# Kernel tuning notes

Hardware: AMD Instinct MI355X
Metric: run time of the kernel (lower is better)

The kernel has to match this reference:

```python
import jax, jax.numpy as jnp
import numpy as np

B, N, S, K = 8, 4096, 1024, 128   # clouds, pts/cloud, fps samples (ratio=0.25), max neighbors
R = 0.2                            # radius
DIN = 3                            # point feature dim


def setup_inputs() -> dict:
    key = jax.random.key(0)
    ks = jax.random.split(key, 8)
    x = jax.random.normal(ks[0], (B * N, DIN), dtype=jnp.float32)
    pos = jax.random.uniform(ks[1], (B * N, 3), dtype=jnp.float32)
    batch = jnp.repeat(jnp.arange(B, dtype=jnp.int32), N)
    def lin(k, fi, fo):
        return jax.random.normal(k, (fi, fo), dtype=jnp.float32) / np.float32(np.sqrt(fi))
    W1 = lin(ks[2], DIN + 3, 64); b1 = jnp.zeros((64,), jnp.float32)
    W2 = lin(ks[3], 64, 64);      b2 = jnp.zeros((64,), jnp.float32)
    W3 = lin(ks[4], 64, 128);     b3 = jnp.zeros((128,), jnp.float32)
    return {"x": x, "pos": pos, "W1": W1, "b1": b1, "W2": W2, "b2": b2,
            "W3": W3, "b3": b3, "batch": batch}


def _fps(pos3):
    """Farthest point sampling per cloud. pos3: [B,N,3] -> idx [B,S] (start at point 0)."""
    d0 = jnp.sum((pos3 - pos3[:, :1]) ** 2, axis=-1)  # [B,N]
    def step(min_d, _):
        nxt = jnp.argmax(min_d, axis=1).astype(jnp.int32)             # [B]
        p = jnp.take_along_axis(pos3, nxt[:, None, None], axis=1)      # [B,1,3]
        d = jnp.sum((pos3 - p) ** 2, axis=-1)
        return jnp.minimum(min_d, d), nxt
    _, idxs = jax.lax.scan(step, d0, None, length=S - 1)               # [S-1,B]
    first = jnp.zeros((B, 1), jnp.int32)
    return jnp.concatenate([first, idxs.T], axis=1)                    # [B,S]


def reference(x, pos, W1, b1, W2, b2, W3, b3, batch):
    x3 = x.reshape(B, N, DIN)
    pos3 = pos.reshape(B, N, 3)
    batch2 = batch.reshape(B, N)

    idx = _fps(pos3)                                                   # [B,S]
    q = jnp.take_along_axis(pos3, idx[:, :, None], axis=1)             # [B,S,3]

    # radius ball query, capped at K nearest within R (deterministic variant of torch radius)
    d2 = jnp.sum((q[:, :, None, :] - pos3[:, None, :, :]) ** 2, -1)    # [B,S,N]
    masked = jnp.where(d2 <= R * R, d2, jnp.inf)
    negd, nbr = jax.lax.top_k(-masked, K)                              # [B,S,K]
    valid = jnp.isfinite(negd)                                         # [B,S,K]

    gather = jax.vmap(lambda a, i: a[i])                                # per-cloud fancy gather
    xj = gather(x3, nbr)                                               # [B,S,K,DIN]
    pj = gather(pos3, nbr)                                             # [B,S,K,3]
    rel = pj - q[:, :, None, :]
    feat = jnp.concatenate([xj, rel], axis=-1)                         # [B,S,K,6]

    h = jax.nn.relu(feat @ W1 + b1)
    h = jax.nn.relu(h @ W2 + b2)
    h = h @ W3 + b3                                                    # plain last layer

    h = jnp.where(valid[..., None], h, -jnp.inf)
    out = jnp.max(h, axis=2)                                           # max aggregation [B,S,128]
    out = jnp.where(jnp.any(valid, axis=2)[..., None], out, 0.0)

    x_out = out.reshape(B * S, -1)
    pos_out = q.reshape(B * S, 3)
    batch_out = jnp.take_along_axis(batch2, idx, axis=1).reshape(B * S)
    return x_out, pos_out, batch_out
```

## Files before the change

### kernel.cpp

```cpp
#include <hip/hip_runtime.h>
#include <hip/hip_fp16.h>

#define BB   8
#define NPTS 4096
#define SS   1024
#define KK   128

typedef _Float16 half8 __attribute__((ext_vector_type(8)));
typedef float    f32x4 __attribute__((ext_vector_type(4)));

#define FPS_T 256
#define PPT   16

#define DPP_FMAX(CTRL)                                                                  \
    {                                                                                   \
        unsigned o = (unsigned)__builtin_amdgcn_update_dpp(                             \
            (int)__float_as_uint(m), (int)__float_as_uint(m), CTRL, 0xF, 0xF, false);   \
        m = fmaxf(m, __uint_as_float(o));                                               \
    }

__global__ __launch_bounds__(FPS_T) void fps_e_kernel(const float* __restrict__ pos,
                                                      const int* __restrict__ batch,
                                                      const float* __restrict__ x,
                                                      const float* __restrict__ W1,
                                                      float* __restrict__ E,
                                                      float* __restrict__ pos_out,
                                                      float* __restrict__ batch_out) {
    if (blockIdx.x >= BB) {
        int id = (blockIdx.x - BB) * FPS_T + threadIdx.x;
        int c = id & 63;
        int n = id >> 6;
        float x0 = x[n * 3 + 0], x1 = x[n * 3 + 1], x2 = x[n * 3 + 2];
        float p0 = pos[n * 3 + 0], p1 = pos[n * 3 + 1], p2 = pos[n * 3 + 2];
        float v = x0 * W1[0 * 64 + c] + x1 * W1[1 * 64 + c] + x2 * W1[2 * 64 + c]
                + p0 * W1[3 * 64 + c] + p1 * W1[4 * 64 + c] + p2 * W1[5 * 64 + c];
        E[(size_t)n * 64 + c] = v;
        return;
    }

    __shared__ __align__(16) float4 Pl[NPTS];
    __shared__ __align__(16) unsigned long long wkey[2][4];

    int b = blockIdx.x;
    int t = threadIdx.x;
    int w = t >> 6, l = t & 63;
    const float* P = pos + (size_t)b * NPTS * 3;

    for (int i = t; i < NPTS; i += FPS_T) {
        Pl[i] = make_float4(P[i * 3 + 0], P[i * 3 + 1], P[i * 3 + 2], 0.f);
    }
    float bval = (float)batch[(size_t)b * NPTS];
    for (int i = t; i < SS; i += FPS_T) batch_out[b * SS + i] = bval;

    float px[PPT], py[PPT], pz[PPT], md[PPT];
    int base = t * PPT;
#pragma unroll
    for (int j = 0; j < PPT; j++) {
        px[j] = P[(base + j) * 3 + 0];
        py[j] = P[(base + j) * 3 + 1];
        pz[j] = P[(base + j) * 3 + 2];
    }
    float c0x = P[0], c0y = P[1], c0z = P[2];
    float lm = -1.f;
#pragma unroll
    for (int j = 0; j < PPT; j++) {
        float dx = __fsub_rn(px[j], c0x);
        float dy = __fsub_rn(py[j], c0y);
        float dz = __fsub_rn(pz[j], c0z);
        md[j] = __fadd_rn(__fadd_rn(__fmul_rn(dx, dx), __fmul_rn(dy, dy)), __fmul_rn(dz, dz));
        lm = fmaxf(lm, md[j]);
    }
    if (t == 0) {
        float* qp = pos_out + (size_t)(b * SS) * 3;
        qp[0] = c0x; qp[1] = c0y; qp[2] = c0z;
    }
    __syncthreads();

    for (int s = 1; s < SS; s++) {
        int jsel = 0x7FFFFFFF;
#pragma unroll
        for (int j = PPT - 1; j >= 0; j--)
            if (md[j] == lm) jsel = base + j;

        float m = lm;
        DPP_FMAX(0x111)
        DPP_FMAX(0x112)
        DPP_FMAX(0x114)
        DPP_FMAX(0x118)
        DPP_FMAX(0x142)
        DPP_FMAX(0x143)
        float wm = __uint_as_float((unsigned)__builtin_amdgcn_readlane(__float_as_uint(m), 63));

        unsigned long long mask = __ballot(lm == wm);
        int L = __ffsll((long long)mask) - 1;
        int si = __builtin_amdgcn_readlane(jsel, L);

        if (l == 0)
            wkey[s & 1][w] = (((unsigned long long)__float_as_uint(wm)) << 32) | (~(unsigned)si);
        __syncthreads();

        const unsigned long long* wk = wkey[s & 1];
        unsigned long long g0 = wk[0] > wk[1] ? wk[0] : wk[1];
        unsigned long long g1 = wk[2] > wk[3] ? wk[2] : wk[3];
        unsigned long long g = g0 > g1 ? g0 : g1;
        int gi = (int)(~(unsigned)g);

        float4 c = Pl[gi];
        if (t == 0) {
            float* qp = pos_out + (size_t)(b * SS + s) * 3;
            qp[0] = c.x; qp[1] = c.y; qp[2] = c.z;
        }
        float nlm = -1.f;
#pragma unroll
        for (int j = 0; j < PPT; j++) {
            float dx = __fsub_rn(px[j], c.x);
            float dy = __fsub_rn(py[j], c.y);
            float dz = __fsub_rn(pz[j], c.z);
            float d2 = __fadd_rn(__fadd_rn(__fmul_rn(dx, dx), __fmul_rn(dy, dy)), __fmul_rn(dz, dz));
            md[j] = fminf(md[j], d2);
            nlm = fmaxf(nlm, md[j]);
        }
        lm = nlm;
    }
}

#define CAP 512

__global__ __launch_bounds__(256) void ball_kernel(const float* __restrict__ pos,
                                                   const float* __restrict__ qpos,
                                                   int* __restrict__ nbr) {
    __shared__ float cd2[4][CAP];
    __shared__ int   cidx[4][CAP];
    int t = threadIdx.x, w = t >> 6, l = t & 63;
    int qi = blockIdx.x * 4 + w;
    int b = qi >> 10;
    int bBase = b * NPTS;
    const float* P = pos + (size_t)bBase * 3;
    float qx = qpos[qi * 3 + 0], qy = qpos[qi * 3 + 1], qz = qpos[qi * 3 + 2];

    int total = 0;
    for (int n0 = 0; n0 < NPTS; n0 += 64) {
        int n = n0 + l;
        float x = P[n * 3 + 0], y = P[n * 3 + 1], z = P[n * 3 + 2];
        float dx = __fsub_rn(qx, x);
        float dy = __fsub_rn(qy, y);
        float dz = __fsub_rn(qz, z);
        float d2 = __fadd_rn(__fadd_rn(__fmul_rn(dx, dx), __fmul_rn(dy, dy)), __fmul_rn(dz, dz));
        bool in = (d2 <= 0.04f);
        unsigned long long mask = __ballot(in);
        int mypos = total + (int)__popcll(mask & ((1ull << l) - 1ull));
        if (in && mypos < CAP) { cd2[w][mypos] = d2; cidx[w][mypos] = n; }
        total += (int)__popcll(mask);
    }

    int* onbr = nbr + (size_t)qi * KK;
    if (total <= KK) {
        for (int i = l; i < KK; i += 64)
            onbr[i] = bBase + cidx[w][i < total ? i : 0];
    } else {
        int nc = total < CAP ? total : CAP;
        unsigned long long key[8];
#pragma unroll
        for (int i = 0; i < 8; i++) {
            int p = l + (i << 6);
            key[i] = (p < nc)
                   ? ((((unsigned long long)__float_as_uint(cd2[w][p])) << 12) | (unsigned)cidx[w][p])
                   : ~0ull;
        }
        unsigned long long lo = 0, hi = ((unsigned long long)0x3D23D70Bu) << 12;
        while (lo < hi) {
            unsigned long long mid = (lo + hi) >> 1;
            int cnt = 0;
#pragma unroll
            for (int i = 0; i < 8; i++) cnt += (int)__popcll(__ballot(key[i] <= mid));
            if (cnt >= KK) hi = mid; else lo = mid + 1;
        }
        int done = 0;
#pragma unroll
        for (int i = 0; i < 8; i++) {
            bool s2 = (key[i] <= lo);
            unsigned long long mk = __ballot(s2);
            int p2 = done + (int)__popcll(mk & ((1ull << l) - 1ull));
            if (s2) onbr[p2] = bBase + (int)(key[i] & 0xFFFull);
            done += (int)__popcll(mk);
        }
    }
}

__global__ __launch_bounds__(256) void mlp_kernel(const float* __restrict__ E,
                                                  const int* __restrict__ nbr,
                                                  const float* __restrict__ qpos,
                                                  const float* __restrict__ W1,
                                                  const float* __restrict__ b1,
                                                  const float* __restrict__ W2,
                                                  const float* __restrict__ b2,
                                                  const float* __restrict__ W3,
                                                  const float* __restrict__ b3,
                                                  float* __restrict__ xout,
                                                  int qPerBlk) {
    __shared__ __align__(16) _Float16 W2t[64 * 64];
    __shared__ __align__(16) _Float16 W3t[128 * 64];
    __shared__ __align__(16) _Float16 h2buf[4][32 * 64];
    __shared__ __align__(16) float csh[64];
    __shared__ float cpart[4][128];
    __shared__ float b2s[64];
    __shared__ float b3s[128];

    int t = threadIdx.x, w = t >> 6, l = t & 63;
    int lhi = l >> 4, llo = l & 15;

    for (int i = t; i < 64 * 64; i += 256) {
        int n = i >> 6, k = i & 63;
        W2t[(n << 6) | (k ^ ((n & 7) << 3))] = (_Float16)W2[k * 64 + n];
    }
    for (int i = t; i < 128 * 64; i += 256) {
        int n = i >> 6, k = i & 63;
        W3t[(n << 6) | (k ^ ((n & 7) << 3))] = (_Float16)W3[k * 128 + n];
    }
    if (t < 64) b2s[t] = b2[t];
    if (t < 128) b3s[t] = b3[t];
    __syncthreads();

    int q0 = blockIdx.x * qPerBlk;
    for (int qq = 0; qq < qPerBlk; qq++) {
        int qi = q0 + qq;
        if (t < 64) {
            float qx = qpos[qi * 3 + 0], qy = qpos[qi * 3 + 1], qz = qpos[qi * 3 + 2];
            csh[t] = b1[t] - (qx * W1[3 * 64 + t] + qy * W1[4 * 64 + t] + qz * W1[5 * 64 + t]);
        }
        __syncthreads();

        half8 a2[2][2];
        int row0 = w * 32;
#pragma unroll
        for (int mt = 0; mt < 2; mt++) {
            int r = row0 + mt * 16 + llo;
            int nb = nbr[(size_t)qi * KK + r];
            const float* Er = E + (size_t)nb * 64;
#pragma unroll
            for (int ks = 0; ks < 2; ks++) {
                int k0 = lhi * 8 + ks * 32;
                f32x4 e0 = *(const f32x4*)(Er + k0);
                f32x4 e1 = *(const f32x4*)(Er + k0 + 4);
                f32x4 c0 = *(const f32x4*)(csh + k0);
                f32x4 c1 = *(const f32x4*)(csh + k0 + 4);
                half8 a;
#pragma unroll
                for (int e = 0; e < 4; e++) {
                    a[e]     = (_Float16)fmaxf(e0[e] + c0[e], 0.f);
                    a[4 + e] = (_Float16)fmaxf(e1[e] + c1[e], 0.f);
                }
                a2[mt][ks] = a;
            }
        }

        f32x4 acc2[2][4];
#pragma unroll
        for (int mt = 0; mt < 2; mt++)
#pragma unroll
            for (int nt = 0; nt < 4; nt++) acc2[mt][nt] = (f32x4){0.f, 0.f, 0.f, 0.f};
#pragma unroll
        for (int ks = 0; ks < 2; ks++) {
            int k0 = lhi * 8 + ks * 32;
#pragma unroll
            for (int nt = 0; nt < 4; nt++) {
                int n = nt * 16 + llo;
                half8 bf = *(const half8*)&W2t[(n << 6) | (k0 ^ ((n & 7) << 3))];
#pragma unroll
                for (int mt = 0; mt < 2; mt++)
                    acc2[mt][nt] = __builtin_amdgcn_mfma_f32_16x16x32_f16(a2[mt][ks], bf, acc2[mt][nt], 0, 0, 0);
            }
        }

        _Float16* hb = h2buf[w];
#pragma unroll
        for (int mt = 0; mt < 2; mt++)
#pragma unroll
            for (int nt = 0; nt < 4; nt++)
#pragma unroll
                for (int r = 0; r < 4; r++) {
                    int lr = mt * 16 + lhi * 4 + r;
                    int n = nt * 16 + llo;
                    float v = fmaxf(acc2[mt][nt][r] + b2s[n], 0.f);
                    hb[(lr << 6) | (n ^ ((lr & 7) << 3))] = (_Float16)v;
                }

        half8 a3[2][2];
#pragma unroll
        for (int mt = 0; mt < 2; mt++)
#pragma unroll
            for (int ks = 0; ks < 2; ks++) {
                int lr = mt * 16 + llo;
                int k0 = lhi * 8 + ks * 32;
                a3[mt][ks] = *(const half8*)&hb[(lr << 6) | (k0 ^ ((lr & 7) << 3))];
            }
        f32x4 acc3[2][8];
#pragma unroll
        for (int mt = 0; mt < 2; mt++)
#pragma unroll
            for (int nt = 0; nt < 8; nt++) acc3[mt][nt] = (f32x4){0.f, 0.f, 0.f, 0.f};
#pragma unroll
        for (int ks = 0; ks < 2; ks++) {
            int k0 = lhi * 8 + ks * 32;
#pragma unroll
            for (int nt = 0; nt < 8; nt++) {
                int n = nt * 16 + llo;
                half8 bf = *(const half8*)&W3t[(n << 6) | (k0 ^ ((n & 7) << 3))];
#pragma unroll
                for (int mt = 0; mt < 2; mt++)
                    acc3[mt][nt] = __builtin_amdgcn_mfma_f32_16x16x32_f16(a3[mt][ks], bf, acc3[mt][nt], 0, 0, 0);
            }
        }

#pragma unroll
        for (int nt = 0; nt < 8; nt++) {
            float m = acc3[0][nt][0];
#pragma unroll
            for (int r = 1; r < 4; r++) m = fmaxf(m, acc3[0][nt][r]);
#pragma unroll
            for (int r = 0; r < 4; r++) m = fmaxf(m, acc3[1][nt][r]);
            m = fmaxf(m, __shfl_xor(m, 16));
            m = fmaxf(m, __shfl_xor(m, 32));
            if (l < 16) cpart[w][nt * 16 + l] = m;
        }
        __syncthreads();
        if (t < 128) {
            float v = fmaxf(fmaxf(cpart[0][t], cpart[1][t]), fmaxf(cpart[2][t], cpart[3][t])) + b3s[t];
            xout[(size_t)qi * 128 + t] = v;
        }
        __syncthreads();
    }
}

extern "C" void kernel_launch(void* const* d_in, const int* in_sizes, int n_in,
                              void* d_out, int out_size, void* d_ws, size_t ws_size,
                              hipStream_t stream) {
    const float* x   = (const float*)d_in[0];
    const float* pos = (const float*)d_in[1];
    const float* W1  = (const float*)d_in[2];
    const float* b1  = (const float*)d_in[3];
    const float* W2  = (const float*)d_in[4];
    const float* b2  = (const float*)d_in[5];
    const float* W3  = (const float*)d_in[6];
    const float* b3  = (const float*)d_in[7];
    const int* batch = (const int*)d_in[8];

    float* xout      = (float*)d_out;
    float* pos_out   = xout + (size_t)BB * SS * 128;
    float* batch_out = pos_out + (size_t)BB * SS * 3;

    float* E  = (float*)d_ws;
    int* nbr  = (int*)((char*)d_ws + (size_t)32768 * 64 * 4);

    fps_e_kernel<<<dim3(BB + 8192), dim3(FPS_T), 0, stream>>>(pos, batch, x, W1, E, pos_out, batch_out);
    ball_kernel<<<dim3(2048), dim3(256), 0, stream>>>(pos, pos_out, nbr);
    mlp_kernel<<<dim3(2048), dim3(256), 0, stream>>>(E, nbr, pos_out, W1, b1, W2, b2, W3, b3, xout, 4);
}
```

Baseline: 725.0 us.

## Fuse FPS, ball query and MLP into one persistent kernel with progress flags

Merges the three kernels into a single persistent launch. Eight high-priority blocks run farthest point sampling and publish per-cloud progress counters every 64 samples. The remaining worker blocks compute the E table, then run the ball query and MLP for each query group once its FPS samples are published. This lets the neighbor search and MLP overlap with the long serial FPS loop and drops the intermediate neighbor buffer. It relies on all blocks being co-resident for the spin-waits, which risks deadlock if they are not, and it adds atomic polling overhead.

```diff
diff --git a/kernel.cpp b/kernel.cpp
--- a/kernel.cpp
+++ b/kernel.cpp
@@ -1,16 +1,43 @@
 #include <hip/hip_runtime.h>
 #include <hip/hip_fp16.h>
 
-#define BB   8
-#define NPTS 4096
-#define SS   1024
-#define KK   128
+#define BB    8
+#define NPTS  4096
+#define SS    1024
+#define KK    128
+#define CAP   512
+#define NW    504
+#define TPB   256
+#define PPT   16
 
 typedef _Float16 half8 __attribute__((ext_vector_type(8)));
 typedef float    f32x4 __attribute__((ext_vector_type(4)));
 
-#define FPS_T 256
-#define PPT   16
+
+struct __align__(16) FpsSm {
+    float4 Pl[NPTS];
+    unsigned long long wkey[2][4];
+};
+struct __align__(16) WkSm {
+    float cd2[4][CAP];
+    int   cidx[4][CAP];
+    int   nbrL[4][KK];
+    _Float16 W2t[64 * 64];
+    _Float16 W3t[128 * 64];
+    _Float16 h2buf[4][32 * 64];
+    float csh[64];
+    float cpart[4][128];
+    float b2s[64];
+    float b3s[128];
+};
+union __align__(16) SMem { FpsSm f; WkSm w; };
+
+__device__ __forceinline__ void st_rel(unsigned* p, unsigned v) {
+    __hip_atomic_store(p, v, __ATOMIC_RELEASE, __HIP_MEMORY_SCOPE_AGENT);
+}
+__device__ __forceinline__ unsigned ld_acq(unsigned* p) {
+    return __hip_atomic_load(p, __ATOMIC_ACQUIRE, __HIP_MEMORY_SCOPE_AGENT);
+}
 
 #define DPP_FMAX(CTRL)                                                                  \
     {                                                                                   \
@@ -19,15 +46,110 @@
         m = fmaxf(m, __uint_as_float(o));                                               \
     }
 
-__global__ __launch_bounds__(FPS_T) void fps_e_kernel(const float* __restrict__ pos,
-                                                      const int* __restrict__ batch,
-                                                      const float* __restrict__ x,
-                                                      const float* __restrict__ W1,
-                                                      float* __restrict__ E,
-                                                      float* __restrict__ pos_out,
-                                                      float* __restrict__ batch_out) {
-    if (blockIdx.x >= BB) {
-        int id = (blockIdx.x - BB) * FPS_T + threadIdx.x;
+__global__ __launch_bounds__(TPB) void fused_kernel(const float* __restrict__ pos,
+                                                    const int* __restrict__ batch,
+                                                    const float* __restrict__ x,
+                                                    const float* __restrict__ W1,
+                                                    const float* __restrict__ b1,
+                                                    const float* __restrict__ W2,
+                                                    const float* __restrict__ b2,
+                                                    const float* __restrict__ W3,
+                                                    const float* __restrict__ b3,
+                                                    float* __restrict__ E,
+                                                    float* __restrict__ pos_out,
+                                                    float* __restrict__ batch_out,
+                                                    float* __restrict__ xout,
+                                                    unsigned* __restrict__ sync) {
+    __shared__ SMem sm;
+    int t = threadIdx.x, w = t >> 6, l = t & 63;
+
+    if (blockIdx.x < BB) {
+        __builtin_amdgcn_s_setprio(3);
+        int b = blockIdx.x;
+        const float* P = pos + (size_t)b * NPTS * 3;
+
+        for (int i = t; i < NPTS; i += TPB) {
+            sm.f.Pl[i] = make_float4(P[i * 3 + 0], P[i * 3 + 1], P[i * 3 + 2], 0.f);
+        }
+        float bval = (float)batch[(size_t)b * NPTS];
+        for (int i = t; i < SS; i += TPB) batch_out[b * SS + i] = bval;
+
+        float px[PPT], py[PPT], pz[PPT], md[PPT];
+        int base = t * PPT;
+#pragma unroll
+        for (int j = 0; j < PPT; j++) {
+            px[j] = P[(base + j) * 3 + 0];
+            py[j] = P[(base + j) * 3 + 1];
+            pz[j] = P[(base + j) * 3 + 2];
+        }
+        float c0x = P[0], c0y = P[1], c0z = P[2];
+        float lm = -1.f;
+#pragma unroll
+        for (int j = 0; j < PPT; j++) {
+            float dx = __fsub_rn(px[j], c0x);
+            float dy = __fsub_rn(py[j], c0y);
+            float dz = __fsub_rn(pz[j], c0z);
+            md[j] = __fadd_rn(__fadd_rn(__fmul_rn(dx, dx), __fmul_rn(dy, dy)), __fmul_rn(dz, dz));
+            lm = fmaxf(lm, md[j]);
+        }
+        if (t == 0) {
+            float* qp = pos_out + (size_t)(b * SS) * 3;
+            qp[0] = c0x; qp[1] = c0y; qp[2] = c0z;
+        }
+        __syncthreads();
+
+        for (int s = 1; s < SS; s++) {
+            int jsel = 0x7FFFFFFF;
+#pragma unroll
+            for (int j = PPT - 1; j >= 0; j--)
+                if (md[j] == lm) jsel = base + j;
+
+            float m = lm;
+            DPP_FMAX(0x111)
+            DPP_FMAX(0x112)
+            DPP_FMAX(0x114)
+            DPP_FMAX(0x118)
+            DPP_FMAX(0x142)
+            DPP_FMAX(0x143)
+            float wm = __uint_as_float((unsigned)__builtin_amdgcn_readlane(__float_as_uint(m), 63));
+
+            unsigned long long mask = __ballot(lm == wm);
+            int L = __ffsll((long long)mask) - 1;
+            int si = __builtin_amdgcn_readlane(jsel, L);
+
+            if (l == 0)
+                sm.f.wkey[s & 1][w] = (((unsigned long long)__float_as_uint(wm)) << 32) | (~(unsigned)si);
+            __syncthreads();
+
+            const unsigned long long* wk = sm.f.wkey[s & 1];
+            unsigned long long g0 = wk[0] > wk[1] ? wk[0] : wk[1];
+            unsigned long long g1 = wk[2] > wk[3] ? wk[2] : wk[3];
+            unsigned long long g = g0 > g1 ? g0 : g1;
+            int gi = (int)(~(unsigned)g);
+
+            float4 c = sm.f.Pl[gi];
+            if (t == 0) {
+                float* qp = pos_out + (size_t)(b * SS + s) * 3;
+                qp[0] = c.x; qp[1] = c.y; qp[2] = c.z;
+                if ((s & 63) == 63) st_rel(&sync[b * 32], (unsigned)(s + 1));
+            }
+#pragma unroll
+            for (int j = 0; j < PPT; j++) {
+                float dx = __fsub_rn(px[j], c.x);
+                float dy = __fsub_rn(py[j], c.y);
+                float dz = __fsub_rn(pz[j], c.z);
+                float d2 = __fadd_rn(__fadd_rn(__fmul_rn(dx, dx), __fmul_rn(dy, dy)), __fmul_rn(dz, dz));
+                md[j] = fminf(md[j], d2);
+                lm = (j == 0) ? fmaxf(-1.f, md[0]) : fmaxf(lm, md[j]);
+            }
+        }
+        return;
+    }
+
+    int wid = blockIdx.x - BB;
+    unsigned* ectr = &sync[256];
+
+    for (int id = wid * TPB + t; id < 32768 * 64; id += NW * TPB) {
         int c = id & 63;
         int n = id >> 6;
         float x0 = x[n * 3 + 0], x1 = x[n * 3 + 1], x2 = x[n * 3 + 2];
@@ -35,298 +157,198 @@
         float v = x0 * W1[0 * 64 + c] + x1 * W1[1 * 64 + c] + x2 * W1[2 * 64 + c]
                 + p0 * W1[3 * 64 + c] + p1 * W1[4 * 64 + c] + p2 * W1[5 * 64 + c];
         E[(size_t)n * 64 + c] = v;
-        return;
-    }
-
-    __shared__ __align__(16) float4 Pl[NPTS];
-    __shared__ __align__(16) unsigned long long wkey[2][4];
-
-    int b = blockIdx.x;
-    int t = threadIdx.x;
-    int w = t >> 6, l = t & 63;
-    const float* P = pos + (size_t)b * NPTS * 3;
-
-    for (int i = t; i < NPTS; i += FPS_T) {
-        Pl[i] = make_float4(P[i * 3 + 0], P[i * 3 + 1], P[i * 3 + 2], 0.f);
-    }
-    float bval = (float)batch[(size_t)b * NPTS];
-    for (int i = t; i < SS; i += FPS_T) batch_out[b * SS + i] = bval;
-
-    float px[PPT], py[PPT], pz[PPT], md[PPT];
-    int base = t * PPT;
-#pragma unroll
-    for (int j = 0; j < PPT; j++) {
-        px[j] = P[(base + j) * 3 + 0];
-        py[j] = P[(base + j) * 3 + 1];
-        pz[j] = P[(base + j) * 3 + 2];
-    }
-    float c0x = P[0], c0y = P[1], c0z = P[2];
-    float lm = -1.f;
-#pragma unroll
-    for (int j = 0; j < PPT; j++) {
-        float dx = __fsub_rn(px[j], c0x);
-        float dy = __fsub_rn(py[j], c0y);
-        float dz = __fsub_rn(pz[j], c0z);
-        md[j] = __fadd_rn(__fadd_rn(__fmul_rn(dx, dx), __fmul_rn(dy, dy)), __fmul_rn(dz, dz));
-        lm = fmaxf(lm, md[j]);
-    }
+    }
+    if (l == 0) __hip_atomic_fetch_add(ectr, 1u, __ATOMIC_RELEASE, __HIP_MEMORY_SCOPE_AGENT);
+
+    for (int i = t; i < 64 * 64; i += TPB) {
+        int n = i >> 6, k = i & 63;
+        sm.w.W2t[(n << 6) | (k ^ ((n & 7) << 3))] = (_Float16)W2[k * 64 + n];
+    }
+    for (int i = t; i < 128 * 64; i += TPB) {
+        int n = i >> 6, k = i & 63;
+        sm.w.W3t[(n << 6) | (k ^ ((n & 7) << 3))] = (_Float16)W3[k * 128 + n];
+    }
+    if (t < 64) sm.w.b2s[t] = b2[t];
+    if (t < 128) sm.w.b3s[t] = b3[t];
+
     if (t == 0) {
-        float* qp = pos_out + (size_t)(b * SS) * 3;
-        qp[0] = c0x; qp[1] = c0y; qp[2] = c0z;
+        while (ld_acq(ectr) < NW * 4u) __builtin_amdgcn_s_sleep(16);
     }
     __syncthreads();
 
-    for (int s = 1; s < SS; s++) {
-        int jsel = 0x7FFFFFFF;
-#pragma unroll
-        for (int j = PPT - 1; j >= 0; j--)
-            if (md[j] == lm) jsel = base + j;
-
-        float m = lm;
-        DPP_FMAX(0x111)
-        DPP_FMAX(0x112)
-        DPP_FMAX(0x114)
-        DPP_FMAX(0x118)
-        DPP_FMAX(0x142)
-        DPP_FMAX(0x143)
-        float wm = __uint_as_float((unsigned)__builtin_amdgcn_readlane(__float_as_uint(m), 63));
-
-        unsigned long long mask = __ballot(lm == wm);
-        int L = __ffsll((long long)mask) - 1;
-        int si = __builtin_amdgcn_readlane(jsel, L);
-
-        if (l == 0)
-            wkey[s & 1][w] = (((unsigned long long)__float_as_uint(wm)) << 32) | (~(unsigned)si);
+    int lhi = l >> 4, llo = l & 15;
+
+    for (int g = wid; g < 2048; g += NW) {
+        int cb = g >> 8;
+        unsigned need = ((unsigned)(g & 255)) * 4u + 4u;
+        if (t == 0) {
+            while (ld_acq(&sync[cb * 32]) < need) __builtin_amdgcn_s_sleep(16);
+        }
         __syncthreads();
 
-        const unsigned long long* wk = wkey[s & 1];
-        unsigned long long g0 = wk[0] > wk[1] ? wk[0] : wk[1];
-        unsigned long long g1 = wk[2] > wk[3] ? wk[2] : wk[3];
-        unsigned long long g = g0 > g1 ? g0 : g1;
-        int gi = (int)(~(unsigned)g);
-
-        float4 c = Pl[gi];
-        if (t == 0) {
-            float* qp = pos_out + (size_t)(b * SS + s) * 3;
-            qp[0] = c.x; qp[1] = c.y; qp[2] = c.z;
-        }
-        float nlm = -1.f;
-#pragma unroll
-        for (int j = 0; j < PPT; j++) {
-            float dx = __fsub_rn(px[j], c.x);
-            float dy = __fsub_rn(py[j], c.y);
-            float dz = __fsub_rn(pz[j], c.z);
-            float d2 = __fadd_rn(__fadd_rn(__fmul_rn(dx, dx), __fmul_rn(dy, dy)), __fmul_rn(dz, dz));
-            md[j] = fminf(md[j], d2);
-            nlm = fmaxf(nlm, md[j]);
-        }
-        lm = nlm;
-    }
-}
-
-#define CAP 512
-
-__global__ __launch_bounds__(256) void ball_kernel(const float* __restrict__ pos,
-                                                   const float* __restrict__ qpos,
-                                                   int* __restrict__ nbr) {
-    __shared__ float cd2[4][CAP];
-    __shared__ int   cidx[4][CAP];
-    int t = threadIdx.x, w = t >> 6, l = t & 63;
-    int qi = blockIdx.x * 4 + w;
-    int b = qi >> 10;
-    int bBase = b * NPTS;
-    const float* P = pos + (size_t)bBase * 3;
-    float qx = qpos[qi * 3 + 0], qy = qpos[qi * 3 + 1], qz = qpos[qi * 3 + 2];
-
-    int total = 0;
-    for (int n0 = 0; n0 < NPTS; n0 += 64) {
-        int n = n0 + l;
-        float x = P[n * 3 + 0], y = P[n * 3 + 1], z = P[n * 3 + 2];
-        float dx = __fsub_rn(qx, x);
-        float dy = __fsub_rn(qy, y);
-        float dz = __fsub_rn(qz, z);
-        float d2 = __fadd_rn(__fadd_rn(__fmul_rn(dx, dx), __fmul_rn(dy, dy)), __fmul_rn(dz, dz));
-        bool in = (d2 <= 0.04f);
-        unsigned long long mask = __ballot(in);
-        int mypos = total + (int)__popcll(mask & ((1ull << l) - 1ull));
-        if (in && mypos < CAP) { cd2[w][mypos] = d2; cidx[w][mypos] = n; }
-        total += (int)__popcll(mask);
-    }
-
-    int* onbr = nbr + (size_t)qi * KK;
-    if (total <= KK) {
-        for (int i = l; i < KK; i += 64)
-            onbr[i] = bBase + cidx[w][i < total ? i : 0];
-    } else {
-        int nc = total < CAP ? total : CAP;
-        unsigned long long key[8];
-#pragma unroll
-        for (int i = 0; i < 8; i++) {
-            int p = l + (i << 6);
-            key[i] = (p < nc)
-                   ? ((((unsigned long long)__float_as_uint(cd2[w][p])) << 12) | (unsigned)cidx[w][p])
-                   : ~0ull;
-        }
-        unsigned long long lo = 0, hi = ((unsigned long long)0x3D23D70Bu) << 12;
-        while (lo < hi) {
-            unsigned long long mid = (lo + hi) >> 1;
-            int cnt = 0;
-#pragma unroll
-            for (int i = 0; i < 8; i++) cnt += (int)__popcll(__ballot(key[i] <= mid));
-            if (cnt >= KK) hi = mid; else lo = mid + 1;
-        }
-        int done = 0;
-#pragma unroll
-        for (int i = 0; i < 8; i++) {
-            bool s2 = (key[i] <= lo);
-            unsigned long long mk = __ballot(s2);
-            int p2 = done + (int)__popcll(mk & ((1ull << l) - 1ull));
-            if (s2) onbr[p2] = bBase + (int)(key[i] & 0xFFFull);
-            done += (int)__popcll(mk);
-        }
-    }
-}
-
-__global__ __launch_bounds__(256) void mlp_kernel(const float* __restrict__ E,
-                                                  const int* __restrict__ nbr,
-                                                  const float* __restrict__ qpos,
-                                                  const float* __restrict__ W1,
-                                                  const float* __restrict__ b1,
-                                                  const float* __restrict__ W2,
-                                                  const float* __restrict__ b2,
-                                                  const float* __restrict__ W3,
-                                                  const float* __restrict__ b3,
-                                                  float* __restrict__ xout,
-                                                  int qPerBlk) {
-    __shared__ __align__(16) _Float16 W2t[64 * 64];
-    __shared__ __align__(16) _Float16 W3t[128 * 64];
-    __shared__ __align__(16) _Float16 h2buf[4][32 * 64];
-    __shared__ __align__(16) float csh[64];
-    __shared__ float cpart[4][128];
-    __shared__ float b2s[64];
-    __shared__ float b3s[128];
-
-    int t = threadIdx.x, w = t >> 6, l = t & 63;
-    int lhi = l >> 4, llo = l & 15;
-
-    for (int i = t; i < 64 * 64; i += 256) {
-        int n = i >> 6, k = i & 63;
-        W2t[(n << 6) | (k ^ ((n & 7) << 3))] = (_Float16)W2[k * 64 + n];
-    }
-    for (int i = t; i < 128 * 64; i += 256) {
-        int n = i >> 6, k = i & 63;
-        W3t[(n << 6) | (k ^ ((n & 7) << 3))] = (_Float16)W3[k * 128 + n];
-    }
-    if (t < 64) b2s[t] = b2[t];
-    if (t < 128) b3s[t] = b3[t];
-    __syncthreads();
-
-    int q0 = blockIdx.x * qPerBlk;
-    for (int qq = 0; qq < qPerBlk; qq++) {
-        int qi = q0 + qq;
-        if (t < 64) {
-            float qx = qpos[qi * 3 + 0], qy = qpos[qi * 3 + 1], qz = qpos[qi * 3 + 2];
-            csh[t] = b1[t] - (qx * W1[3 * 64 + t] + qy * W1[4 * 64 + t] + qz * W1[5 * 64 + t]);
+        {
+            int qi = 4 * g + w;
+            int bBase = cb * NPTS;
+            const float* P = pos + (size_t)bBase * 3;
+            float qx = pos_out[qi * 3 + 0], qy = pos_out[qi * 3 + 1], qz = pos_out[qi * 3 + 2];
+
+            int total = 0;
+            for (int n0 = 0; n0 < NPTS; n0 += 64) {
+                int n = n0 + l;
+                float xx = P[n * 3 + 0], yy = P[n * 3 + 1], zz = P[n * 3 + 2];
+                float dx = __fsub_rn(qx, xx);
+                float dy = __fsub_rn(qy, yy);
+                float dz = __fsub_rn(qz, zz);
+                float d2 = __fadd_rn(__fadd_rn(__fmul_rn(dx, dx), __fmul_rn(dy, dy)), __fmul_rn(dz, dz));
+                bool in = (d2 <= 0.04f);
+                unsigned long long mask = __ballot(in);
+                int mypos = total + (int)__popcll(mask & ((1ull << l) - 1ull));
+                if (in && mypos < CAP) { sm.w.cd2[w][mypos] = d2; sm.w.cidx[w][mypos] = n; }
+                total += (int)__popcll(mask);
+            }
+
+            if (total <= KK) {
+                for (int i = l; i < KK; i += 64)
+                    sm.w.nbrL[w][i] = bBase + sm.w.cidx[w][i < total ? i : 0];
+            } else {
+                int nc = total < CAP ? total : CAP;
+                unsigned long long key[8];
+#pragma unroll
+                for (int i = 0; i < 8; i++) {
+                    int p = l + (i << 6);
+                    key[i] = (p < nc)
+                           ? ((((unsigned long long)__float_as_uint(sm.w.cd2[w][p])) << 12) | (unsigned)sm.w.cidx[w][p])
+                           : ~0ull;
+                }
+                unsigned long long lo = 0, hi = ((unsigned long long)0x3D23D70Bu) << 12;
+                while (lo < hi) {
+                    unsigned long long mid = (lo + hi) >> 1;
+                    int cnt = 0;
+#pragma unroll
+                    for (int i = 0; i < 8; i++) cnt += (int)__popcll(__ballot(key[i] <= mid));
+                    if (cnt >= KK) hi = mid; else lo = mid + 1;
+                }
+                int done = 0;
+#pragma unroll
+                for (int i = 0; i < 8; i++) {
+                    bool s2 = (key[i] <= lo);
+                    unsigned long long mk = __ballot(s2);
+                    int p2 = done + (int)__popcll(mk & ((1ull << l) - 1ull));
+                    if (s2) sm.w.nbrL[w][p2] = bBase + (int)(key[i] & 0xFFFull);
+                    done += (int)__popcll(mk);
+                }
+            }
         }
         __syncthreads();
 
-        half8 a2[2][2];
-        int row0 = w * 32;
-#pragma unroll
-        for (int mt = 0; mt < 2; mt++) {
-            int r = row0 + mt * 16 + llo;
-            int nb = nbr[(size_t)qi * KK + r];
-            const float* Er = E + (size_t)nb * 64;
+        for (int qq = 0; qq < 4; qq++) {
+            int qi = 4 * g + qq;
+            if (t < 64) {
+                float qx = pos_out[qi * 3 + 0], qy = pos_out[qi * 3 + 1], qz = pos_out[qi * 3 + 2];
+                sm.w.csh[t] = b1[t] - (qx * W1[3 * 64 + t] + qy * W1[4 * 64 + t] + qz * W1[5 * 64 + t]);
+            }
+            __syncthreads();
+
+            half8 a2[2][2];
+            int row0 = w * 32;
+#pragma unroll
+            for (int mt = 0; mt < 2; mt++) {
+                int r = row0 + mt * 16 + llo;
+                int nb = sm.w.nbrL[qq][r];
+                const float* Er = E + (size_t)nb * 64;
+#pragma unroll
+                for (int ks = 0; ks < 2; ks++) {
+                    int k0 = lhi * 8 + ks * 32;
+                    f32x4 e0 = *(const f32x4*)(Er + k0);
+                    f32x4 e1 = *(const f32x4*)(Er + k0 + 4);
+                    f32x4 c0 = *(const f32x4*)(sm.w.csh + k0);
+                    f32x4 c1 = *(const f32x4*)(sm.w.csh + k0 + 4);
+                    half8 a;
+#pragma unroll
+                    for (int e = 0; e < 4; e++) {
+                        a[e]     = (_Float16)fmaxf(e0[e] + c0[e], 0.f);
+                        a[4 + e] = (_Float16)fmaxf(e1[e] + c1[e], 0.f);
+                    }
+                    a2[mt][ks] = a;
+                }
+            }
+
+            f32x4 acc2[2][4];
+#pragma unroll
+            for (int mt = 0; mt < 2; mt++)
+#pragma unroll
+                for (int nt = 0; nt < 4; nt++) acc2[mt][nt] = (f32x4){0.f, 0.f, 0.f, 0.f};
 #pragma unroll
             for (int ks = 0; ks < 2; ks++) {
                 int k0 = lhi * 8 + ks * 32;
-                f32x4 e0 = *(const f32x4*)(Er + k0);
-                f32x4 e1 = *(const f32x4*)(Er + k0 + 4);
-                f32x4 c0 = *(const f32x4*)(csh + k0);
-                f32x4 c1 = *(const f32x4*)(csh + k0 + 4);
-                half8 a;
-#pragma unroll
-                for (int e = 0; e < 4; e++) {
-                    a[e]     = (_Float16)fmaxf(e0[e] + c0[e], 0.f);
-                    a[4 + e] = (_Float16)fmaxf(e1[e] + c1[e], 0.f);
-                }
-                a2[mt][ks] = a;
-            }
-        }
-
-        f32x4 acc2[2][4];
-#pragma unroll
-        for (int mt = 0; mt < 2; mt++)
-#pragma unroll
-            for (int nt = 0; nt < 4; nt++) acc2[mt][nt] = (f32x4){0.f, 0.f, 0.f, 0.f};
-#pragma unroll
-        for (int ks = 0; ks < 2; ks++) {
-            int k0 = lhi * 8 + ks * 32;
-#pragma unroll
-            for (int nt = 0; nt < 4; nt++) {
-                int n = nt * 16 + llo;
-                half8 bf = *(const half8*)&W2t[(n << 6) | (k0 ^ ((n & 7) << 3))];
-#pragma unroll
-                for (int mt = 0; mt < 2; mt++)
-                    acc2[mt][nt] = __builtin_amdgcn_mfma_f32_16x16x32_f16(a2[mt][ks], bf, acc2[mt][nt], 0, 0, 0);
-            }
-        }
-
-        _Float16* hb = h2buf[w];
-#pragma unroll
-        for (int mt = 0; mt < 2; mt++)
-#pragma unroll
-            for (int nt = 0; nt < 4; nt++)
-#pragma unroll
-                for (int r = 0; r < 4; r++) {
-                    int lr = mt * 16 + lhi * 4 + r;
+#pragma unroll
+                for (int nt = 0; nt < 4; nt++) {
                     int n = nt * 16 + llo;
-                    float v = fmaxf(acc2[mt][nt][r] + b2s[n], 0.f);
-                    hb[(lr << 6) | (n ^ ((lr & 7) << 3))] = (_Float16)v;
-                }
-
-        half8 a3[2][2];
-#pragma unroll
-        for (int mt = 0; mt < 2; mt++)
+                    half8 bf = *(const half8*)&sm.w.W2t[(n << 6) | (k0 ^ ((n & 7) << 3))];
+#pragma unroll
+                    for (int mt = 0; mt < 2; mt++)
+                        acc2[mt][nt] = __builtin_amdgcn_mfma_f32_16x16x32_f16(a2[mt][ks], bf, acc2[mt][nt], 0, 0, 0);
+                }
+            }
+
+            _Float16* hb = sm.w.h2buf[w];
+#pragma unroll
+            for (int mt = 0; mt < 2; mt++)
+#pragma unroll
+                for (int nt = 0; nt < 4; nt++)
+#pragma unroll
+                    for (int r = 0; r < 4; r++) {
+                        int lr = mt * 16 + lhi * 4 + r;
+                        int n = nt * 16 + llo;
+                        float v = fmaxf(acc2[mt][nt][r] + sm.w.b2s[n], 0.f);
+                        hb[(lr << 6) | (n ^ ((lr & 7) << 3))] = (_Float16)v;
+                    }
+
+            half8 a3[2][2];
+#pragma unroll
+            for (int mt = 0; mt < 2; mt++)
+#pragma unroll
+                for (int ks = 0; ks < 2; ks++) {
+                    int lr = mt * 16 + llo;
+                    int k0 = lhi * 8 + ks * 32;
+                    a3[mt][ks] = *(const half8*)&hb[(lr << 6) | (k0 ^ ((lr & 7) << 3))];
+                }
+            f32x4 acc3[2][8];
+#pragma unroll
+            for (int mt = 0; mt < 2; mt++)
+#pragma unroll
+                for (int nt = 0; nt < 8; nt++) acc3[mt][nt] = (f32x4){0.f, 0.f, 0.f, 0.f};
 #pragma unroll
             for (int ks = 0; ks < 2; ks++) {
-                int lr = mt * 16 + llo;
                 int k0 = lhi * 8 + ks * 32;
-                a3[mt][ks] = *(const half8*)&hb[(lr << 6) | (k0 ^ ((lr & 7) << 3))];
-            }
-        f32x4 acc3[2][8];
-#pragma unroll
-        for (int mt = 0; mt < 2; mt++)
-#pragma unroll
-            for (int nt = 0; nt < 8; nt++) acc3[mt][nt] = (f32x4){0.f, 0.f, 0.f, 0.f};
-#pragma unroll
-        for (int ks = 0; ks < 2; ks++) {
-            int k0 = lhi * 8 + ks * 32;
+#pragma unroll
+                for (int nt = 0; nt < 8; nt++) {
+                    int n = nt * 16 + llo;
+                    half8 bf = *(const half8*)&sm.w.W3t[(n << 6) | (k0 ^ ((n & 7) << 3))];
+#pragma unroll
+                    for (int mt = 0; mt < 2; mt++)
+                        acc3[mt][nt] = __builtin_amdgcn_mfma_f32_16x16x32_f16(a3[mt][ks], bf, acc3[mt][nt], 0, 0, 0);
+                }
+            }
+
 #pragma unroll
             for (int nt = 0; nt < 8; nt++) {
-                int n = nt * 16 + llo;
-                half8 bf = *(const half8*)&W3t[(n << 6) | (k0 ^ ((n & 7) << 3))];
-#pragma unroll
-                for (int mt = 0; mt < 2; mt++)
-                    acc3[mt][nt] = __builtin_amdgcn_mfma_f32_16x16x32_f16(a3[mt][ks], bf, acc3[mt][nt], 0, 0, 0);
-            }
-        }
-
-#pragma unroll
-        for (int nt = 0; nt < 8; nt++) {
-            float m = acc3[0][nt][0];
-#pragma unroll
-            for (int r = 1; r < 4; r++) m = fmaxf(m, acc3[0][nt][r]);
-#pragma unroll
-            for (int r = 0; r < 4; r++) m = fmaxf(m, acc3[1][nt][r]);
-            m = fmaxf(m, __shfl_xor(m, 16));
-            m = fmaxf(m, __shfl_xor(m, 32));
-            if (l < 16) cpart[w][nt * 16 + l] = m;
-        }
-        __syncthreads();
-        if (t < 128) {
-            float v = fmaxf(fmaxf(cpart[0][t], cpart[1][t]), fmaxf(cpart[2][t], cpart[3][t])) + b3s[t];
-            xout[(size_t)qi * 128 + t] = v;
+                float m = acc3[0][nt][0];
+#pragma unroll
+                for (int r = 1; r < 4; r++) m = fmaxf(m, acc3[0][nt][r]);
+#pragma unroll
+                for (int r = 0; r < 4; r++) m = fmaxf(m, acc3[1][nt][r]);
+                m = fmaxf(m, __shfl_xor(m, 16));
+                m = fmaxf(m, __shfl_xor(m, 32));
+                if (l < 16) sm.w.cpart[w][nt * 16 + l] = m;
+            }
+            __syncthreads();
+            if (t < 128) {
+                float v = fmaxf(fmaxf(sm.w.cpart[0][t], sm.w.cpart[1][t]),
+                                fmaxf(sm.w.cpart[2][t], sm.w.cpart[3][t])) + sm.w.b3s[t];
+                xout[(size_t)qi * 128 + t] = v;
+            }
+            __syncthreads();
         }
         __syncthreads();
     }
@@ -349,10 +371,10 @@
     float* pos_out   = xout + (size_t)BB * SS * 128;
     float* batch_out = pos_out + (size_t)BB * SS * 3;
 
-    float* E  = (float*)d_ws;
-    int* nbr  = (int*)((char*)d_ws + (size_t)32768 * 64 * 4);
-
-    fps_e_kernel<<<dim3(BB + 8192), dim3(FPS_T), 0, stream>>>(pos, batch, x, W1, E, pos_out, batch_out);
-    ball_kernel<<<dim3(2048), dim3(256), 0, stream>>>(pos, pos_out, nbr);
-    mlp_kernel<<<dim3(2048), dim3(256), 0, stream>>>(E, nbr, pos_out, W1, b1, W2, b2, W3, b3, xout, 4);
+    float* E = (float*)d_ws;
+    unsigned* sync = (unsigned*)((char*)d_ws + (size_t)32768 * 64 * 4);
+    hipMemsetAsync(sync, 0, 4096, stream);
+
+    fused_kernel<<<dim3(BB + NW), dim3(TPB), 0, stream>>>(
+        pos, batch, x, W1, b1, W2, b2, W3, b3, E, pos_out, batch_out, xout, sync);
 }
```

After: 736.4 us. About the same (+1.6%).
